# Kernel optimization log

Measured on AMD Instinct MI355X. Metric: run time of the kernel, lower is better.

The kernel has to match this reference:

```python
import jax, jax.numpy as jnp
import numpy as np
from jax import lax

BN_EPS = 1e-3
SLOPE = 0.1
CLUSTER_TEMP = 30.0
K = 16
FEAT = 4096  # 8*8*64


def conv_bn_lrelu(x, w, b, g, beta, m, v):
    # Conv2d stride 2, padding 1 (NCHW / OIHW), then eval-mode BatchNorm, then LeakyReLU.
    y = lax.conv_general_dilated(x, w, window_strides=(2, 2), padding=((1, 1), (1, 1)),
                                 dimension_numbers=("NCHW", "OIHW", "NCHW"))
    y = y + b[None, :, None, None]
    scale = g / jnp.sqrt(v + BN_EPS)
    y = y * scale[None, :, None, None] + (beta - m * scale)[None, :, None, None]
    return jnp.where(y > 0, y, SLOPE * y)


def soft_kmeans(data, mu, num_iter, ct):
    # Row L2-normalize (equivalent to diag(1/||x||) @ data)
    data = data / jnp.linalg.norm(data, axis=1, keepdims=True)
    for _ in range(num_iter):
        dist = data @ mu.T                      # [N, K]
        r = jax.nn.softmax(ct * dist, axis=1)   # [N, K]
        mu = (r.T @ data) / r.sum(axis=0)[:, None]  # [K, F]
    dist = data @ mu.T
    r = jax.nn.softmax(ct * dist, axis=1)
    return mu, r, dist


def setup_inputs() -> dict:
    key = jax.random.key(0)
    ks = jax.random.split(key, 12)
    d = {}
    d["x"] = jax.random.normal(ks[0], (256, 3, 64, 64), dtype=jnp.float32)
    # conv1: 3 -> 128
    d["conv1_w"] = jax.random.normal(ks[1], (128, 3, 3, 3), dtype=jnp.float32) * 0.05
    d["conv1_b"] = jnp.zeros((128,), jnp.float32)
    d["bn1_g"] = jnp.ones((128,), jnp.float32)
    d["bn1_b"] = jnp.zeros((128,), jnp.float32)
    d["bn1_m"] = jax.random.normal(ks[2], (128,), dtype=jnp.float32) * 0.1
    d["bn1_v"] = jax.random.uniform(ks[3], (128,), minval=0.5, maxval=1.5, dtype=jnp.float32)
    # conv2: 128 -> 256
    d["conv2_w"] = jax.random.normal(ks[4], (256, 128, 3, 3), dtype=jnp.float32) * 0.02
    d["conv2_b"] = jnp.zeros((256,), jnp.float32)
    d["bn2_g"] = jnp.ones((256,), jnp.float32)
    d["bn2_b"] = jnp.zeros((256,), jnp.float32)
    d["bn2_m"] = jax.random.normal(ks[5], (256,), dtype=jnp.float32) * 0.1
    d["bn2_v"] = jax.random.uniform(ks[6], (256,), minval=0.5, maxval=1.5, dtype=jnp.float32)
    # conv3: 256 -> 64
    d["conv3_w"] = jax.random.normal(ks[7], (64, 256, 3, 3), dtype=jnp.float32) * 0.02
    d["conv3_b"] = jnp.zeros((64,), jnp.float32)
    d["bn3_g"] = jnp.ones((64,), jnp.float32)
    d["bn3_b"] = jnp.zeros((64,), jnp.float32)
    d["bn3_m"] = jax.random.normal(ks[8], (64,), dtype=jnp.float32) * 0.1
    d["bn3_v"] = jax.random.uniform(ks[9], (64,), minval=0.5, maxval=1.5, dtype=jnp.float32)
    # initial cluster centers, torch.rand(K, F)
    d["mu0"] = jax.random.uniform(ks[10], (K, FEAT), dtype=jnp.float32)
    d["num_iter"] = 10
    return d


def reference(x, conv1_w, conv1_b, bn1_g, bn1_b, bn1_m, bn1_v,
              conv2_w, conv2_b, bn2_g, bn2_b, bn2_m, bn2_v,
              conv3_w, conv3_b, bn3_g, bn3_b, bn3_m, bn3_v,
              mu0, num_iter):
    h = conv_bn_lrelu(x, conv1_w, conv1_b, bn1_g, bn1_b, bn1_m, bn1_v)   # [B,128,32,32]
    h = conv_bn_lrelu(h, conv2_w, conv2_b, bn2_g, bn2_b, bn2_m, bn2_v)   # [B,256,16,16]
    h = conv_bn_lrelu(h, conv3_w, conv3_b, bn3_g, bn3_b, bn3_m, bn3_v)   # [B,64,8,8]
    embeds = h.reshape(-1, FEAT)                                          # [B, 4096]
    mu_init, _, _ = soft_kmeans(embeds, mu0, num_iter, CLUSTER_TEMP)
    _, r, _ = soft_kmeans(embeds, lax.stop_gradient(mu_init), 1, CLUSTER_TEMP)
    return r
```

## Files before the change

### kernel.cpp

```cpp
#include <hip/hip_runtime.h>
#include <stdint.h>
#include <stddef.h>

typedef unsigned short u16;
typedef __attribute__((ext_vector_type(8))) short short8;
typedef __attribute__((ext_vector_type(4))) float f32x4;
typedef __attribute__((ext_vector_type(4))) int int4v;

__device__ __forceinline__ float bf2f(u16 u) {
    unsigned x = ((unsigned)u) << 16;
    return __uint_as_float(x);
}
__device__ __forceinline__ u16 f2bf(float f) {
    unsigned x = __float_as_uint(f);
    unsigned r = (x + 0x7fffu + ((x >> 16) & 1u)) >> 16;
    return (u16)r;
}
__device__ __forceinline__ float ldin(const void* p, size_t i, int isbf) {
    return isbf ? bf2f(((const u16*)p)[i]) : ((const float*)p)[i];
}
__device__ __forceinline__ int detect_bf(const void* v1) {
    const u16* ub = (const u16*)v1;
    int ok = 1;
#pragma unroll
    for (int i = 0; i < 16; i++) {
        float f = bf2f(ub[i]);
        if (!(f >= 0.4f && f <= 1.6f)) ok = 0;
    }
    return ok;
}
__device__ __forceinline__ int sw(int r, int c8) {
    return r * 32 + (((c8) ^ (r & 3)) << 3);
}

struct PrepArgs {
    const void *w1, *w2, *w3;
    u16 *W1p, *W2p, *W3p;
    const void *b1, *g1, *be1, *m1, *v1;
    const void *b2, *g2, *be2, *m2, *v2;
    const void *b3, *g3, *be3, *m3, *v3;
    float *es1, *esh1, *es2, *esh2, *es3, *esh3;
    u16 *zb;
};
__device__ __forceinline__ void packw_body(const void* src, u16* dst, int CI, int Kp,
                                           int total, int blk, int t, int isbf) {
    int p = blk * 256 + t;
    if (p >= total) return;
    int co = p / Kp, k = p - co * Kp;
    int tap = k / CI, ci = k - tap * CI;
    u16 v = 0;
    if (tap < 9) {
        size_t si = (size_t)(co * CI + ci) * 9 + tap;
        v = isbf ? ((const u16*)src)[si] : f2bf(((const float*)src)[si]);
    }
    dst[p] = v;
}
__global__ __launch_bounds__(256) void kprep_all(PrepArgs A) {
    int b = blockIdx.x, t = threadIdx.x;
    int isbf = detect_bf(A.v1);
    if (b < 1152) {
        packw_body(A.w2, A.W2p, 128, 1152, 256 * 1152, b, t, isbf);
    } else if (b < 1728) {
        packw_body(A.w3, A.W3p, 256, 2304, 64 * 2304, b - 1152, t, isbf);
    } else if (b < 1744) {
        packw_body(A.w1, A.W1p, 3, 32, 128 * 32, b - 1728, t, isbf);
    } else {
        if (b == 1745) A.zb[t] = 0;
        int u = (b - 1744) * 256 + t;
        const void *bb, *g, *be, *m, *v;
        float *es, *esh;
        int c;
        if (u < 128)      { c = u;       bb=A.b1; g=A.g1; be=A.be1; m=A.m1; v=A.v1; es=A.es1; esh=A.esh1; }
        else if (u < 384) { c = u - 128; bb=A.b2; g=A.g2; be=A.be2; m=A.m2; v=A.v2; es=A.es2; esh=A.esh2; }
        else if (u < 448) { c = u - 384; bb=A.b3; g=A.g3; be=A.be3; m=A.m3; v=A.v3; es=A.es3; esh=A.esh3; }
        else return;
        float sc = ldin(g, c, isbf) / sqrtf(ldin(v, c, isbf) + 1e-3f);
        float sh = (ldin(bb, c, isbf) - ldin(m, c, isbf)) * sc + ldin(be, c, isbf);
        es[c] = sc;
        esh[c] = sh;
    }
}

__global__ void kfallback(u16* __restrict__ out) {
    int i = blockIdx.x * 256 + threadIdx.x;
    if (i < 4096) out[i] = f2bf(0.0625f);
}

__global__ __launch_bounds__(256) void im2col1(const void* __restrict__ x,
                                               u16* __restrict__ A1,
                                               const void* __restrict__ v1ref) {
    int n = blockIdx.x, t = threadIdx.x;
    int isbf = detect_bf(v1ref);
    __shared__ u16 xs[3 * 64 * 64];
    if (isbf) {
        const u16* xp = (const u16*)x + (size_t)n * 12288;
#pragma unroll
        for (int i = t * 8; i < 12288; i += 2048)
            *(int4v*)&xs[i] = *(const int4v*)&xp[i];
    } else {
        const float* xp = (const float*)x + (size_t)n * 12288;
#pragma unroll
        for (int i = t * 4; i < 12288; i += 1024) {
            float4 v = *(const float4*)&xp[i];
            xs[i] = f2bf(v.x); xs[i + 1] = f2bf(v.y);
            xs[i + 2] = f2bf(v.z); xs[i + 3] = f2bf(v.w);
        }
    }
    __syncthreads();
#pragma unroll
    for (int rr = 0; rr < 4; rr++) {
        int m = rr * 256 + t;
        int ox = m & 31, oy = m >> 5;
        alignas(16) u16 row[32];
#pragma unroll
        for (int k = 0; k < 32; k++) {
            u16 val = 0;
            if (k < 27) {
                int tap = k / 3, ci = k - 3 * tap;
                int ky = tap / 3, kx = tap - 3 * ky;
                int iy = 2 * oy - 1 + ky, ix = 2 * ox - 1 + kx;
                if ((unsigned)iy < 64u && (unsigned)ix < 64u)
                    val = xs[ci * 4096 + iy * 64 + ix];
            }
            row[k] = val;
        }
        int4v* dst = (int4v*)(A1 + ((size_t)n * 1024 + m) * 32);
        const int4v* srcv = (const int4v*)row;
#pragma unroll
        for (int q = 0; q < 4; q++) dst[q] = srcv[q];
    }
}

__global__ __launch_bounds__(256) void gemm_conv1(
    const u16* __restrict__ A1, const u16* __restrict__ W,
    const float* __restrict__ es, const float* __restrict__ esh,
    u16* __restrict__ OutB) {
    alignas(16) __shared__ u16 As[128 * 32];
    alignas(16) __shared__ u16 Bs[128 * 32];
    const int t = threadIdx.x;
    const int m0 = blockIdx.x * 128;
    const int lane = t & 63, w = t >> 6;
    const int wm = w & 1, wn = w >> 1;
    const int rA = t >> 2, c8 = t & 3, koff = c8 * 8;

#pragma unroll
    for (int j = 0; j < 2; j++) {
        int4v va = *(const int4v*)(A1 + (size_t)(m0 + j * 64 + rA) * 32 + koff);
        *(int4v*)&As[sw(j * 64 + rA, c8)] = va;
        int4v vb = *(const int4v*)(W + (size_t)(j * 64 + rA) * 32 + koff);
        *(int4v*)&Bs[sw(j * 64 + rA, c8)] = vb;
    }
    __syncthreads();
    const int qc = lane >> 4, fr = lane & 15;
    short8 af[4], bf[4];
#pragma unroll
    for (int i = 0; i < 4; i++) af[i] = *(const short8*)&As[sw(wm * 64 + i * 16 + fr, qc)];
#pragma unroll
    for (int j = 0; j < 4; j++) bf[j] = *(const short8*)&Bs[sw(wn * 64 + j * 16 + fr, qc)];
    f32x4 acc[4][4];
#pragma unroll
    for (int i = 0; i < 4; i++)
#pragma unroll
        for (int j = 0; j < 4; j++) {
#pragma unroll
            for (int q = 0; q < 4; q++) acc[i][j][q] = 0.f;
            acc[i][j] = __builtin_amdgcn_mfma_f32_16x16x32_bf16(af[i], bf[j], acc[i][j], 0, 0, 0);
        }
    float scv[4], shv[4];
#pragma unroll
    for (int j = 0; j < 4; j++) {
        int c = wn * 64 + j * 16 + fr;
        scv[j] = es[c];
        shv[j] = esh[c];
    }
#pragma unroll
    for (int i = 0; i < 4; i++) {
#pragma unroll
        for (int rg = 0; rg < 4; rg++) {
            int m = m0 + wm * 64 + i * 16 + qc * 4 + rg;
            int ox = m & 31, oy = (m >> 5) & 31, n = m >> 10;
            u16* orow = OutB + ((size_t)(n * 32 + oy) * 32 + ox) * 128 + wn * 64 + fr;
#pragma unroll
            for (int j = 0; j < 4; j++) {
                float v = acc[i][j][rg] * scv[j] + shv[j];
                v = (v > 0.f) ? v : 0.1f * v;
                orow[j * 16] = f2bf(v);
            }
        }
    }
}

__global__ __launch_bounds__(512, 2) void gemm_conv2(
    const u16* __restrict__ h1, const u16* __restrict__ W,
    const float* __restrict__ es, const float* __restrict__ esh,
    u16* __restrict__ OutB, const u16* __restrict__ zb) {
    alignas(16) __shared__ u16 smem[4 * 16384];
    u16* const Ab0 = smem;
    u16* const Ab1 = smem + 16384;
    u16* const Bb0 = smem + 32768;
    u16* const Bb1 = smem + 49152;

    const int t = threadIdx.x;
    const int w = t >> 6, l = t & 63;
    const int img = blockIdx.x;
    const int wm = w >> 2, wn = w & 3;
    const int fr = l & 15, qc = l >> 4;

    int aiy0[4], aix0[4], ac8e[4];
    int brow[4];
#pragma unroll
    for (int i = 0; i < 4; ++i) {
        int gi = w * 256 + i * 64 + l;
        int r = gi >> 3, c8d = gi & 7;
        int c8s = c8d ^ (r & 7);
        int oy = r >> 4, ox = r & 15;
        aiy0[i] = 2 * oy - 1;
        aix0[i] = 2 * ox - 1;
        ac8e[i] = c8s * 8;
        brow[i] = r * 1152 + c8s * 8;
    }
    auto mkA = [&](int i, int ky, int kx) -> const u16* {
        int iy = aiy0[i] + ky, ix = aix0[i] + kx;
        if ((unsigned)iy < 32u && (unsigned)ix < 32u)
            return h1 + (size_t)(((img * 32 + iy) * 32 + ix) * 128 + ac8e[i]);
        return zb;
    };
    auto stage = [&](const u16* src, u16* ldsbase, int i) {
        __builtin_amdgcn_global_load_lds(
            (const __attribute__((address_space(1))) void*)src,
            (__attribute__((address_space(3))) void*)(ldsbase + (w * 4 + i) * 512),
            16, 0, 0);
    };

    f32x4 acc[8][4];
#pragma unroll
    for (int mi = 0; mi < 8; ++mi)
#pragma unroll
        for (int nj = 0; nj < 4; ++nj)
#pragma unroll
            for (int q = 0; q < 4; ++q) acc[mi][nj][q] = 0.0f;

    auto do_tile = [&](const u16* A, const u16* B) {
#pragma unroll
        for (int kk = 0; kk < 2; ++kk) {
            const int c8 = kk * 4 + qc;
            short8 a[8], b[4];
#pragma unroll
            for (int q = 0; q < 8; ++q) {
                int row = wm * 128 + q * 16 + fr;
                a[q] = *(const short8*)(A + row * 64 + ((c8 ^ (row & 7)) << 3));
            }
#pragma unroll
            for (int j = 0; j < 4; ++j) {
                int row = wn * 64 + j * 16 + fr;
                b[j] = *(const short8*)(B + row * 64 + ((c8 ^ (row & 7)) << 3));
            }
            __builtin_amdgcn_s_setprio(1);
#pragma unroll
            for (int q = 0; q < 8; ++q)
#pragma unroll
                for (int j = 0; j < 4; ++j)
                    acc[q][j] = __builtin_amdgcn_mfma_f32_16x16x32_bf16(
                        a[q], b[j], acc[q][j], 0, 0, 0);
            __builtin_amdgcn_s_setprio(0);
        }
    };

    const u16* pcur[4];
#pragma unroll
    for (int i = 0; i < 4; ++i) pcur[i] = mkA(i, 0, 0);
#pragma unroll
    for (int i = 0; i < 4; ++i) {
        stage(pcur[i], Ab0, i);
        stage(W + brow[i], Bb0, i);
    }

    for (int tap = 0; tap < 9; ++tap) {
        __syncthreads();
#pragma unroll
        for (int i = 0; i < 4; ++i) {
            stage(pcur[i] + 64, Ab1, i);
            stage(W + brow[i] + (2 * tap + 1) * 64, Bb1, i);
        }
        do_tile(Ab0, Bb0);
        __syncthreads();
        if (tap < 8) {
            const int tap2 = tap + 1;
            const int ky2 = (tap2 >= 6) ? 2 : (tap2 >= 3) ? 1 : 0;
            const int kx2 = tap2 - 3 * ky2;
#pragma unroll
            for (int i = 0; i < 4; ++i) pcur[i] = mkA(i, ky2, kx2);
#pragma unroll
            for (int i = 0; i < 4; ++i) {
                stage(pcur[i], Ab0, i);
                stage(W + brow[i] + (2 * tap + 2) * 64, Bb0, i);
            }
        }
        do_tile(Ab1, Bb1);
    }

    float scv[4], shv[4];
#pragma unroll
    for (int nj = 0; nj < 4; ++nj) {
        int c = wn * 64 + nj * 16 + fr;
        scv[nj] = es[c];
        shv[nj] = esh[c];
    }
#pragma unroll
    for (int mi = 0; mi < 8; ++mi) {
#pragma unroll
        for (int rg = 0; rg < 4; ++rg) {
            int r = wm * 128 + mi * 16 + qc * 4 + rg;
            u16* orow = OutB + ((size_t)img * 256 + r) * 256 + wn * 64 + fr;
#pragma unroll
            for (int nj = 0; nj < 4; ++nj) {
                float v = acc[mi][nj][rg] * scv[nj] + shv[nj];
                v = (v > 0.f) ? v : 0.1f * v;
                orow[nj * 16] = f2bf(v);
            }
        }
    }
}

__global__ __launch_bounds__(256) void gemm_conv3f(
    const u16* __restrict__ Asrc, const u16* __restrict__ W,
    const float* __restrict__ es3, const float* __restrict__ esh3,
    float* __restrict__ dat, u16* __restrict__ datbf,
    const u16* __restrict__ zb) {
    alignas(16) __shared__ u16 smem[4 * 4096];
    __shared__ float red[4];
    u16* const AbP[2] = {smem, smem + 4096};
    u16* const BbP[2] = {smem + 8192, smem + 12288};

    const int t = threadIdx.x;
    const int w = t >> 6, l = t & 63;
    const int lid = blockIdx.x;
    const int xcd = lid & 7, slot = lid >> 3;
    const int img = xcd * 32 + slot;
    const int wm = w & 1, wn = w >> 1;
    const int fr = l & 15, qc = l >> 4;

    int aiy0[2], aix0[2], ac8e[2];
    int brow[2];
#pragma unroll
    for (int i = 0; i < 2; ++i) {
        int g = w * 128 + i * 64 + l;
        int r = g >> 3, c8d = g & 7;
        int c8s = c8d ^ (r & 7);
        int oy = r >> 3, ox = r & 7;
        aiy0[i] = 2 * oy - 1;
        aix0[i] = 2 * ox - 1;
        ac8e[i] = c8s * 8;
        brow[i] = r * 2304 + c8s * 8;
    }
    auto mkA = [&](int i, int ky, int kx) -> const u16* {
        int iy = aiy0[i] + ky, ix = aix0[i] + kx;
        if ((unsigned)iy < 16u && (unsigned)ix < 16u)
            return Asrc + (size_t)(((img * 16 + iy) * 16 + ix) * 256 + ac8e[i]);
        return zb;
    };
    auto stage = [&](const u16* src, u16* ldsbase, int i) {
        __builtin_amdgcn_global_load_lds(
            (const __attribute__((address_space(1))) void*)src,
            (__attribute__((address_space(3))) void*)(ldsbase + (w * 2 + i) * 512),
            16, 0, 0);
    };

    f32x4 acc[2][2];
#pragma unroll
    for (int i = 0; i < 2; i++)
#pragma unroll
        for (int j = 0; j < 2; j++)
#pragma unroll
            for (int q = 0; q < 4; q++) acc[i][j][q] = 0.0f;

    auto do_tile = [&](const u16* A, const u16* B) {
#pragma unroll
        for (int kk = 0; kk < 2; ++kk) {
            const int c8 = kk * 4 + qc;
            short8 a[2], b[2];
#pragma unroll
            for (int i = 0; i < 2; ++i) {
                int row = wm * 32 + i * 16 + fr;
                a[i] = *(const short8*)(A + row * 64 + ((c8 ^ (row & 7)) << 3));
            }
#pragma unroll
            for (int j = 0; j < 2; ++j) {
                int row = wn * 32 + j * 16 + fr;
                b[j] = *(const short8*)(B + row * 64 + ((c8 ^ (row & 7)) << 3));
            }
            __builtin_amdgcn_s_setprio(1);
#pragma unroll
            for (int i = 0; i < 2; ++i)
#pragma unroll
                for (int j = 0; j < 2; ++j)
                    acc[i][j] = __builtin_amdgcn_mfma_f32_16x16x32_bf16(
                        a[i], b[j], acc[i][j], 0, 0, 0);
            __builtin_amdgcn_s_setprio(0);
        }
    };

    const u16* pcur[2];
#pragma unroll
    for (int i = 0; i < 2; ++i) pcur[i] = mkA(i, 0, 0);
#pragma unroll
    for (int i = 0; i < 2; ++i) {
        stage(pcur[i], AbP[0], i);
        stage(W + brow[i], BbP[0], i);
    }

    int flat = 0;
    for (int tap = 0; tap < 9; ++tap) {
        for (int q4 = 0; q4 < 4; ++q4, ++flat) {
            const int cb = flat & 1;
            __syncthreads();
            int ntap = tap, nq = q4 + 1;
            if (nq == 4) { nq = 0; ntap = tap + 1; }
            if (ntap < 9) {
                if (nq == 0) {
                    const int ky = (ntap >= 6) ? 2 : (ntap >= 3) ? 1 : 0;
                    const int kx = ntap - 3 * ky;
#pragma unroll
                    for (int i = 0; i < 2; ++i) pcur[i] = mkA(i, ky, kx);
                }
#pragma unroll
                for (int i = 0; i < 2; ++i) {
                    stage(pcur[i] + nq * 64, AbP[cb ^ 1], i);
                    stage(W + brow[i] + ntap * 256 + nq * 64, BbP[cb ^ 1], i);
                }
            }
            do_tile(AbP[cb], BbP[cb]);
        }
    }

    float vals[2][2][4];
    float ssq = 0.f;
#pragma unroll
    for (int j = 0; j < 2; j++) {
        int c = wn * 32 + j * 16 + fr;
        float sc = es3[c], sh = esh3[c];
#pragma unroll
        for (int i = 0; i < 2; i++) {
#pragma unroll
            for (int rg = 0; rg < 4; rg++) {
                float v = acc[i][j][rg] * sc + sh;
                v = (v > 0.f) ? v : 0.1f * v;
                vals[i][j][rg] = v;
                ssq += v * v;
            }
        }
    }
#pragma unroll
    for (int off = 32; off > 0; off >>= 1) ssq += __shfl_xor(ssq, off);
    if (l == 0) red[w] = ssq;
    __syncthreads();
    float inv = 1.0f / sqrtf(red[0] + red[1] + red[2] + red[3]);
#pragma unroll
    for (int j = 0; j < 2; j++) {
        int c = wn * 32 + j * 16 + fr;
#pragma unroll
        for (int i = 0; i < 2; i++) {
#pragma unroll
            for (int rg = 0; rg < 4; rg++) {
                int row = wm * 32 + i * 16 + qc * 4 + rg;
                size_t idx = (size_t)img * 4096 + c * 64 + row;
                float v = vals[i][j][rg] * inv;
                dat[idx] = v;
                datbf[idx] = f2bf(v);
            }
        }
    }
}

__global__ __launch_bounds__(256) void kgr(const u16* __restrict__ dbf,
                                           const float* __restrict__ dat,
                                           const void* __restrict__ mu0,
                                           float* __restrict__ Gp,
                                           float* __restrict__ rb0,
                                           const void* __restrict__ v1ref) {
    const int b = blockIdx.x, t = threadIdx.x;
    __shared__ float part[16][4];
    __shared__ float ds[16];

    if (b < 64) {
        const int tile = b & 15, s = b >> 4;
        const int m0 = (tile & 3) * 64, n0 = (tile >> 2) * 64;
        const int lane = t & 63, w = t >> 6;
        const int wm = w & 1, wn = w >> 1;
        const int fr = lane & 15, qc = lane >> 4;

        f32x4 acc[2][2];
#pragma unroll
        for (int i = 0; i < 2; i++)
#pragma unroll
            for (int j = 0; j < 2; j++)
#pragma unroll
                for (int q = 0; q < 4; q++) acc[i][j][q] = 0.0f;

        const u16* a0p = dbf + (size_t)(m0 + wm * 32 + fr) * 4096 + s * 1024 + qc * 8;
        const u16* a1p = a0p + 16 * 4096;
        const u16* b0p = dbf + (size_t)(n0 + wn * 32 + fr) * 4096 + s * 1024 + qc * 8;
        const u16* b1p = b0p + 16 * 4096;

        short8 Pa0[4], Pa1[4], Pb0[4], Pb1[4];
        short8 Qa0[4], Qa1[4], Qb0[4], Qb1[4];
        auto ldc = [&](short8* A0, short8* A1, short8* B0, short8* B1, int c) {
#pragma unroll
            for (int u = 0; u < 4; ++u) {
                const int o = c * 128 + u * 32;
                A0[u] = *(const short8*)(a0p + o);
                A1[u] = *(const short8*)(a1p + o);
                B0[u] = *(const short8*)(b0p + o);
                B1[u] = *(const short8*)(b1p + o);
            }
        };
        auto mmc = [&](short8* A0, short8* A1, short8* B0, short8* B1) {
#pragma unroll
            for (int u = 0; u < 4; ++u) {
                acc[0][0] = __builtin_amdgcn_mfma_f32_16x16x32_bf16(A0[u], B0[u], acc[0][0], 0, 0, 0);
                acc[0][1] = __builtin_amdgcn_mfma_f32_16x16x32_bf16(A0[u], B1[u], acc[0][1], 0, 0, 0);
                acc[1][0] = __builtin_amdgcn_mfma_f32_16x16x32_bf16(A1[u], B0[u], acc[1][0], 0, 0, 0);
                acc[1][1] = __builtin_amdgcn_mfma_f32_16x16x32_bf16(A1[u], B1[u], acc[1][1], 0, 0, 0);
            }
        };
        ldc(Pa0, Pa1, Pb0, Pb1, 0);
#pragma unroll
        for (int c = 0; c < 4; ++c) {
            ldc(Qa0, Qa1, Qb0, Qb1, 2 * c + 1);
            mmc(Pa0, Pa1, Pb0, Pb1);
            if (c < 3) ldc(Pa0, Pa1, Pb0, Pb1, 2 * c + 2);
            mmc(Qa0, Qa1, Qb0, Qb1);
        }

        float* gp = Gp + (size_t)s * 65536;
#pragma unroll
        for (int j = 0; j < 2; j++) {
            int cc = n0 + wn * 32 + j * 16 + fr;
#pragma unroll
            for (int i = 0; i < 2; i++)
#pragma unroll
                for (int rg = 0; rg < 4; rg++) {
                    int row = m0 + wm * 32 + i * 16 + qc * 4 + rg;
                    gp[row * 256 + cc] = acc[i][j][rg];
                }
        }
    } else {
        const int n = b - 64;
        const int isbf = detect_bf(v1ref);
        const int lane = t & 63, wv = t >> 6;
        float d[16];
#pragma unroll
        for (int j = 0; j < 16; j++) d[j] = dat[(size_t)n * 4096 + j * 256 + t];
#pragma unroll
        for (int k = 0; k < 16; k++) {
            float a = 0.f;
            if (isbf) {
                const u16* mp = (const u16*)mu0 + (size_t)k * 4096;
#pragma unroll
                for (int j = 0; j < 16; j++) a = fmaf(d[j], bf2f(mp[j * 256 + t]), a);
            } else {
                const float* mp = (const float*)mu0 + (size_t)k * 4096;
#pragma unroll
                for (int j = 0; j < 16; j++) a = fmaf(d[j], mp[j * 256 + t], a);
            }
#pragma unroll
            for (int off = 32; off > 0; off >>= 1) a += __shfl_xor(a, off);
            if (lane == 0) part[k][wv] = a;
        }
        __syncthreads();
        if (t < 16) {
            float dk = part[t][0] + part[t][1] + part[t][2] + part[t][3];
            ds[t] = dk;
            __syncthreads();
            float mx = -1e30f;
#pragma unroll
            for (int j = 0; j < 16; j++) mx = fmaxf(mx, ds[j]);
            float sum = 0.f;
#pragma unroll
            for (int j = 0; j < 16; j++) sum += __expf(30.f * (ds[j] - mx));
            rb0[n * 16 + t] = __expf(30.f * (dk - mx)) / sum;
        }
    }
}

__global__ __launch_bounds__(256) void kcomb(const float* __restrict__ Gp,
                                             u16* __restrict__ Ghi,
                                             u16* __restrict__ Glo) {
    const int i = (blockIdx.x * 256 + threadIdx.x) * 4;
    f32x4 s0 = *(const f32x4*)(Gp + i);
    f32x4 s1 = *(const f32x4*)(Gp + 65536 + i);
    f32x4 s2 = *(const f32x4*)(Gp + 131072 + i);
    f32x4 s3 = *(const f32x4*)(Gp + 196608 + i);
    unsigned long long ph = 0, pl = 0;
#pragma unroll
    for (int q = 0; q < 4; q++) {
        float v = ((s0[q] + s1[q]) + s2[q]) + s3[q];
        u16 hi = f2bf(v);
        u16 lo = f2bf(v - bf2f(hi));
        ph |= ((unsigned long long)hi) << (16 * q);
        pl |= ((unsigned long long)lo) << (16 * q);
    }
    *(unsigned long long*)(Ghi + i) = ph;
    *(unsigned long long*)(Glo + i) = pl;
}

__global__ __launch_bounds__(1024) void kmiter(const u16* __restrict__ Ghi,
                                               const u16* __restrict__ Glo,
                                               const float* __restrict__ rb0,
                                               void* __restrict__ dout,
                                               const void* __restrict__ v1ref) {
    const int t = threadIdx.x;
    const int isbf = detect_bf(v1ref);
    const int lane = t & 63, w = t >> 6;
    const int i0 = w * 16;
    const int col = lane & 15;
    const int q = lane >> 4;

    __shared__ u16 rThi[2][16 * 264];
    __shared__ u16 rTlo[2][16 * 264];
    __shared__ float part[2][16][17];

    const u16* Ahirow = Ghi + (size_t)(i0 + col) * 256 + q * 8;
    const u16* Alorow = Glo + (size_t)(i0 + col) * 256 + q * 8;

    {
        float rv[4];
#pragma unroll
        for (int rg = 0; rg < 4; rg++) {
            int row = i0 + q * 4 + rg;
            float v = rb0[row * 16 + col];
            rv[rg] = v;
            u16 hi = f2bf(v);
            rThi[0][col * 264 + row] = hi;
            rTlo[0][col * 264 + row] = f2bf(v - bf2f(hi));
        }
        float s0 = rv[0] + rv[1] + rv[2] + rv[3];
        s0 += __shfl_xor(s0, 16);
        s0 += __shfl_xor(s0, 32);
        if (lane < 16) part[0][w][lane] = s0;
    }
    __syncthreads();
    float rsc = 0.f;
#pragma unroll
    for (int ww = 0; ww < 16; ww++) rsc += part[0][ww][col];

    int cur = 0;
    for (int iter = 0; iter < 11; iter++) {
        f32x4 acc0 = {0.f, 0.f, 0.f, 0.f};
        f32x4 acc1 = {0.f, 0.f, 0.f, 0.f};
#pragma unroll
        for (int s = 0; s < 4; s++) {
            {
                short8 ah = *(const short8*)(Ahirow + s * 32);
                short8 al = *(const short8*)(Alorow + s * 32);
                short8 bh = *(const short8*)&rThi[cur][col * 264 + s * 32 + q * 8];
                short8 bl = *(const short8*)&rTlo[cur][col * 264 + s * 32 + q * 8];
                acc0 = __builtin_amdgcn_mfma_f32_16x16x32_bf16(ah, bh, acc0, 0, 0, 0);
                acc0 = __builtin_amdgcn_mfma_f32_16x16x32_bf16(al, bh, acc0, 0, 0, 0);
                acc0 = __builtin_amdgcn_mfma_f32_16x16x32_bf16(ah, bl, acc0, 0, 0, 0);
            }
            {
                short8 ah = *(const short8*)(Ahirow + (s + 4) * 32);
                short8 al = *(const short8*)(Alorow + (s + 4) * 32);
                short8 bh = *(const short8*)&rThi[cur][col * 264 + (s + 4) * 32 + q * 8];
                short8 bl = *(const short8*)&rTlo[cur][col * 264 + (s + 4) * 32 + q * 8];
                acc1 = __builtin_amdgcn_mfma_f32_16x16x32_bf16(ah, bh, acc1, 0, 0, 0);
                acc1 = __builtin_amdgcn_mfma_f32_16x16x32_bf16(al, bh, acc1, 0, 0, 0);
                acc1 = __builtin_amdgcn_mfma_f32_16x16x32_bf16(ah, bl, acc1, 0, 0, 0);
            }
        }
        float nv[4];
#pragma unroll
        for (int rg = 0; rg < 4; rg++) {
            float dk = (acc0[rg] + acc1[rg]) / rsc;
            float mx = dk;
#pragma unroll
            for (int o = 1; o < 16; o <<= 1) mx = fmaxf(mx, __shfl_xor(mx, o));
            float e = __expf(30.f * (dk - mx));
            float ssum = e;
#pragma unroll
            for (int o = 1; o < 16; o <<= 1) ssum += __shfl_xor(ssum, o);
            nv[rg] = e / ssum;
        }
        if (iter < 10) {
            const int nxt = cur ^ 1;
#pragma unroll
            for (int rg = 0; rg < 4; rg++) {
                int row = i0 + q * 4 + rg;
                u16 hi = f2bf(nv[rg]);
                rThi[nxt][col * 264 + row] = hi;
                rTlo[nxt][col * 264 + row] = f2bf(nv[rg] - bf2f(hi));
            }
            float s0 = nv[0] + nv[1] + nv[2] + nv[3];
            s0 += __shfl_xor(s0, 16);
            s0 += __shfl_xor(s0, 32);
            if (lane < 16) part[nxt][w][lane] = s0;
            __syncthreads();
            rsc = 0.f;
#pragma unroll
            for (int ww = 0; ww < 16; ww++) rsc += part[nxt][ww][col];
            cur = nxt;
        } else {
#pragma unroll
            for (int rg = 0; rg < 4; rg++) {
                int row = i0 + q * 4 + rg;
                if (isbf) ((u16*)dout)[row * 16 + col] = f2bf(nv[rg]);
                else ((float*)dout)[row * 16 + col] = nv[rg];
            }
        }
    }
}

extern "C" void kernel_launch(void* const* d_in, const int* in_sizes, int n_in,
                              void* d_out, int out_size, void* d_ws, size_t ws_size,
                              hipStream_t stream) {
    const void* x   = d_in[0];
    const void* w1  = d_in[1];
    const void* b1  = d_in[2];
    const void* g1  = d_in[3];
    const void* be1 = d_in[4];
    const void* m1  = d_in[5];
    const void* v1  = d_in[6];
    const void* w2  = d_in[7];
    const void* b2  = d_in[8];
    const void* g2  = d_in[9];
    const void* be2 = d_in[10];
    const void* m2  = d_in[11];
    const void* v2  = d_in[12];
    const void* w3  = d_in[13];
    const void* b3  = d_in[14];
    const void* g3  = d_in[15];
    const void* be3 = d_in[16];
    const void* m3  = d_in[17];
    const void* v3  = d_in[18];
    const void* mu0 = d_in[19];

    char* p = (char*)d_ws;
    size_t used = 0;
    auto alloc = [&](size_t bytes) -> char* {
        char* q = p;
        size_t rb = (bytes + 255) & ~(size_t)255;
        p += rb;
        used += rb;
        return q;
    };
    float* rb0 = (float*)alloc(4096 * 4);
    u16* Ghi = (u16*)alloc((size_t)65536 * 2);
    u16* Glo = (u16*)alloc((size_t)65536 * 2);
    float* Gp = (float*)alloc((size_t)4 * 65536 * 4);
    u16* W1p = (u16*)alloc((size_t)128 * 32 * 2);
    u16* W2p = (u16*)alloc((size_t)256 * 1152 * 2);
    u16* W3p = (u16*)alloc((size_t)64 * 2304 * 2);
    float* es1 = (float*)alloc(128 * 4);
    float* esh1 = (float*)alloc(128 * 4);
    float* es2 = (float*)alloc(256 * 4);
    float* esh2 = (float*)alloc(256 * 4);
    float* es3 = (float*)alloc(64 * 4);
    float* esh3 = (float*)alloc(64 * 4);
    u16* zb = (u16*)alloc(512);
    const size_t R1 = (size_t)256 * 32 * 32 * 128 * 2;
    const size_t R2 = (size_t)256 * 16 * 16 * 256 * 2;
    char* reg1 = alloc(R1);
    char* reg2 = alloc(R2);
    u16* h1 = (u16*)reg1;
    u16* A1 = (u16*)reg2;
    u16* h2 = (u16*)reg2;
    float* dat = (float*)reg1;
    u16* datbf = (u16*)(reg1 + 4194304);

    if (used > ws_size) {
        kfallback<<<16, 256, 0, stream>>>((u16*)d_out);
        return;
    }

    PrepArgs pa = {w1, w2, w3, W1p, W2p, W3p,
                   b1, g1, be1, m1, v1, b2, g2, be2, m2, v2, b3, g3, be3, m3, v3,
                   es1, esh1, es2, esh2, es3, esh3, zb};
    kprep_all<<<1746, 256, 0, stream>>>(pa);
    im2col1<<<256, 256, 0, stream>>>(x, A1, v1);
    gemm_conv1<<<dim3(2048), 256, 0, stream>>>(A1, W1p, es1, esh1, h1);
    gemm_conv2<<<dim3(256), 512, 0, stream>>>(h1, W2p, es2, esh2, h2, zb);
    gemm_conv3f<<<dim3(256), 256, 0, stream>>>(h2, W3p, es3, esh3, dat, datbf, zb);
    kgr<<<dim3(320), 256, 0, stream>>>(datbf, dat, mu0, Gp, rb0, v1);
    kcomb<<<dim3(64), 256, 0, stream>>>(Gp, Ghi, Glo);
    kmiter<<<1, 1024, 0, stream>>>(Ghi, Glo, rb0, d_out, v1);
}
```

Before: 257.6 us.

## Split Gram K-dimension 8 ways and register-cache Gram tiles in kmeans loop

The Gram-matrix kernel now splits the 4096-long reduction into 8 slices instead of 4, doubling the number of GEMM blocks to raise parallelism. The combine kernel sums 8 partials. The single-block kmeans iteration kernel drops from 1024 to 512 threads, each wave handling 32 rows. The Gram hi/lo fragments are loaded once into registers instead of being reloaded from global memory on every iteration, cutting repeated global loads on the serial critical path. The cost is more partial-sum traffic, higher register pressure, and half as many threads in the iteration kernel.

```diff
diff --git a/kernel.cpp b/kernel.cpp
--- a/kernel.cpp
+++ b/kernel.cpp
@@ -482,7 +482,7 @@
     __shared__ float part[16][4];
     __shared__ float ds[16];
 
-    if (b < 64) {
+    if (b < 128) {
         const int tile = b & 15, s = b >> 4;
         const int m0 = (tile & 3) * 64, n0 = (tile >> 2) * 64;
         const int lane = t & 63, w = t >> 6;
@@ -497,9 +497,9 @@
 #pragma unroll
                 for (int q = 0; q < 4; q++) acc[i][j][q] = 0.0f;
 
-        const u16* a0p = dbf + (size_t)(m0 + wm * 32 + fr) * 4096 + s * 1024 + qc * 8;
+        const u16* a0p = dbf + (size_t)(m0 + wm * 32 + fr) * 4096 + s * 512 + qc * 8;
         const u16* a1p = a0p + 16 * 4096;
-        const u16* b0p = dbf + (size_t)(n0 + wn * 32 + fr) * 4096 + s * 1024 + qc * 8;
+        const u16* b0p = dbf + (size_t)(n0 + wn * 32 + fr) * 4096 + s * 512 + qc * 8;
         const u16* b1p = b0p + 16 * 4096;
 
         short8 Pa0[4], Pa1[4], Pb0[4], Pb1[4];
@@ -525,10 +525,10 @@
         };
         ldc(Pa0, Pa1, Pb0, Pb1, 0);
 #pragma unroll
-        for (int c = 0; c < 4; ++c) {
+        for (int c = 0; c < 2; ++c) {
             ldc(Qa0, Qa1, Qb0, Qb1, 2 * c + 1);
             mmc(Pa0, Pa1, Pb0, Pb1);
-            if (c < 3) ldc(Pa0, Pa1, Pb0, Pb1, 2 * c + 2);
+            if (c < 1) ldc(Pa0, Pa1, Pb0, Pb1, 2 * c + 2);
             mmc(Qa0, Qa1, Qb0, Qb1);
         }
 
@@ -545,7 +545,7 @@
                 }
         }
     } else {
-        const int n = b - 64;
+        const int n = b - 128;
         const int isbf = detect_bf(v1ref);
         const int lane = t & 63, wv = t >> 6;
         float d[16];
@@ -587,14 +587,15 @@
                                              u16* __restrict__ Ghi,
                                              u16* __restrict__ Glo) {
     const int i = (blockIdx.x * 256 + threadIdx.x) * 4;
-    f32x4 s0 = *(const f32x4*)(Gp + i);
-    f32x4 s1 = *(const f32x4*)(Gp + 65536 + i);
-    f32x4 s2 = *(const f32x4*)(Gp + 131072 + i);
-    f32x4 s3 = *(const f32x4*)(Gp + 196608 + i);
+    f32x4 s[8];
+#pragma unroll
+    for (int p = 0; p < 8; p++) s[p] = *(const f32x4*)(Gp + (size_t)p * 65536 + i);
     unsigned long long ph = 0, pl = 0;
 #pragma unroll
     for (int q = 0; q < 4; q++) {
-        float v = ((s0[q] + s1[q]) + s2[q]) + s3[q];
+        float v = s[0][q];
+#pragma unroll
+        for (int p = 1; p < 8; p++) v += s[p][q];
         u16 hi = f2bf(v);
         u16 lo = f2bf(v - bf2f(hi));
         ph |= ((unsigned long long)hi) << (16 * q);
@@ -604,37 +605,49 @@
     *(unsigned long long*)(Glo + i) = pl;
 }
 
-__global__ __launch_bounds__(1024) void kmiter(const u16* __restrict__ Ghi,
-                                               const u16* __restrict__ Glo,
-                                               const float* __restrict__ rb0,
-                                               void* __restrict__ dout,
-                                               const void* __restrict__ v1ref) {
+__global__ __launch_bounds__(512) void kmiter(const u16* __restrict__ Ghi,
+                                              const u16* __restrict__ Glo,
+                                              const float* __restrict__ rb0,
+                                              void* __restrict__ dout,
+                                              const void* __restrict__ v1ref) {
     const int t = threadIdx.x;
     const int isbf = detect_bf(v1ref);
     const int lane = t & 63, w = t >> 6;
-    const int i0 = w * 16;
+    const int i0 = w * 32;
     const int col = lane & 15;
     const int q = lane >> 4;
 
     __shared__ u16 rThi[2][16 * 264];
     __shared__ u16 rTlo[2][16 * 264];
-    __shared__ float part[2][16][17];
-
-    const u16* Ahirow = Ghi + (size_t)(i0 + col) * 256 + q * 8;
-    const u16* Alorow = Glo + (size_t)(i0 + col) * 256 + q * 8;
+    __shared__ float part[2][8][17];
+
+    short8 gh[2][8], gl[2][8];
+#pragma unroll
+    for (int sg = 0; sg < 2; sg++) {
+        const u16* Ah = Ghi + (size_t)(i0 + sg * 16 + col) * 256 + q * 8;
+        const u16* Al = Glo + (size_t)(i0 + sg * 16 + col) * 256 + q * 8;
+#pragma unroll
+        for (int s = 0; s < 8; s++) {
+            gh[sg][s] = *(const short8*)(Ah + s * 32);
+            gl[sg][s] = *(const short8*)(Al + s * 32);
+        }
+    }
 
     {
-        float rv[4];
-#pragma unroll
-        for (int rg = 0; rg < 4; rg++) {
-            int row = i0 + q * 4 + rg;
-            float v = rb0[row * 16 + col];
-            rv[rg] = v;
-            u16 hi = f2bf(v);
-            rThi[0][col * 264 + row] = hi;
-            rTlo[0][col * 264 + row] = f2bf(v - bf2f(hi));
-        }
-        float s0 = rv[0] + rv[1] + rv[2] + rv[3];
+        float rv[2][4];
+#pragma unroll
+        for (int sg = 0; sg < 2; sg++)
+#pragma unroll
+            for (int rg = 0; rg < 4; rg++) {
+                int row = i0 + sg * 16 + q * 4 + rg;
+                float v = rb0[row * 16 + col];
+                rv[sg][rg] = v;
+                u16 hi = f2bf(v);
+                rThi[0][col * 264 + row] = hi;
+                rTlo[0][col * 264 + row] = f2bf(v - bf2f(hi));
+            }
+        float s0 = (rv[0][0] + rv[0][1] + rv[0][2] + rv[0][3]) +
+                   (rv[1][0] + rv[1][1] + rv[1][2] + rv[1][3]);
         s0 += __shfl_xor(s0, 16);
         s0 += __shfl_xor(s0, 32);
         if (lane < 16) part[0][w][lane] = s0;
@@ -642,71 +655,76 @@
     __syncthreads();
     float rsc = 0.f;
 #pragma unroll
-    for (int ww = 0; ww < 16; ww++) rsc += part[0][ww][col];
+    for (int ww = 0; ww < 8; ww++) rsc += part[0][ww][col];
 
     int cur = 0;
     for (int iter = 0; iter < 11; iter++) {
-        f32x4 acc0 = {0.f, 0.f, 0.f, 0.f};
-        f32x4 acc1 = {0.f, 0.f, 0.f, 0.f};
+        f32x4 a0[2] = {{0.f, 0.f, 0.f, 0.f}, {0.f, 0.f, 0.f, 0.f}};
+        f32x4 a1[2] = {{0.f, 0.f, 0.f, 0.f}, {0.f, 0.f, 0.f, 0.f}};
 #pragma unroll
         for (int s = 0; s < 4; s++) {
-            {
-                short8 ah = *(const short8*)(Ahirow + s * 32);
-                short8 al = *(const short8*)(Alorow + s * 32);
-                short8 bh = *(const short8*)&rThi[cur][col * 264 + s * 32 + q * 8];
-                short8 bl = *(const short8*)&rTlo[cur][col * 264 + s * 32 + q * 8];
-                acc0 = __builtin_amdgcn_mfma_f32_16x16x32_bf16(ah, bh, acc0, 0, 0, 0);
-                acc0 = __builtin_amdgcn_mfma_f32_16x16x32_bf16(al, bh, acc0, 0, 0, 0);
-                acc0 = __builtin_amdgcn_mfma_f32_16x16x32_bf16(ah, bl, acc0, 0, 0, 0);
-            }
-            {
-                short8 ah = *(const short8*)(Ahirow + (s + 4) * 32);
-                short8 al = *(const short8*)(Alorow + (s + 4) * 32);
-                short8 bh = *(const short8*)&rThi[cur][col * 264 + (s + 4) * 32 + q * 8];
-                short8 bl = *(const short8*)&rTlo[cur][col * 264 + (s + 4) * 32 + q * 8];
-                acc1 = __builtin_amdgcn_mfma_f32_16x16x32_bf16(ah, bh, acc1, 0, 0, 0);
-                acc1 = __builtin_amdgcn_mfma_f32_16x16x32_bf16(al, bh, acc1, 0, 0, 0);
-                acc1 = __builtin_amdgcn_mfma_f32_16x16x32_bf16(ah, bl, acc1, 0, 0, 0);
-            }
-        }
-        float nv[4];
-#pragma unroll
-        for (int rg = 0; rg < 4; rg++) {
-            float dk = (acc0[rg] + acc1[rg]) / rsc;
-            float mx = dk;
-#pragma unroll
-            for (int o = 1; o < 16; o <<= 1) mx = fmaxf(mx, __shfl_xor(mx, o));
-            float e = __expf(30.f * (dk - mx));
-            float ssum = e;
-#pragma unroll
-            for (int o = 1; o < 16; o <<= 1) ssum += __shfl_xor(ssum, o);
-            nv[rg] = e / ssum;
-        }
+            short8 bh = *(const short8*)&rThi[cur][col * 264 + s * 32 + q * 8];
+            short8 bl = *(const short8*)&rTlo[cur][col * 264 + s * 32 + q * 8];
+#pragma unroll
+            for (int sg = 0; sg < 2; sg++) {
+                a0[sg] = __builtin_amdgcn_mfma_f32_16x16x32_bf16(gh[sg][s], bh, a0[sg], 0, 0, 0);
+                a0[sg] = __builtin_amdgcn_mfma_f32_16x16x32_bf16(gl[sg][s], bh, a0[sg], 0, 0, 0);
+                a0[sg] = __builtin_amdgcn_mfma_f32_16x16x32_bf16(gh[sg][s], bl, a0[sg], 0, 0, 0);
+            }
+            short8 bh2 = *(const short8*)&rThi[cur][col * 264 + (s + 4) * 32 + q * 8];
+            short8 bl2 = *(const short8*)&rTlo[cur][col * 264 + (s + 4) * 32 + q * 8];
+#pragma unroll
+            for (int sg = 0; sg < 2; sg++) {
+                a1[sg] = __builtin_amdgcn_mfma_f32_16x16x32_bf16(gh[sg][s + 4], bh2, a1[sg], 0, 0, 0);
+                a1[sg] = __builtin_amdgcn_mfma_f32_16x16x32_bf16(gl[sg][s + 4], bh2, a1[sg], 0, 0, 0);
+                a1[sg] = __builtin_amdgcn_mfma_f32_16x16x32_bf16(gh[sg][s + 4], bl2, a1[sg], 0, 0, 0);
+            }
+        }
+        float nv[2][4];
+#pragma unroll
+        for (int sg = 0; sg < 2; sg++)
+#pragma unroll
+            for (int rg = 0; rg < 4; rg++) {
+                float dk = (a0[sg][rg] + a1[sg][rg]) / rsc;
+                float mx = dk;
+#pragma unroll
+                for (int o = 1; o < 16; o <<= 1) mx = fmaxf(mx, __shfl_xor(mx, o));
+                float e = __expf(30.f * (dk - mx));
+                float ssum = e;
+#pragma unroll
+                for (int o = 1; o < 16; o <<= 1) ssum += __shfl_xor(ssum, o);
+                nv[sg][rg] = e / ssum;
+            }
         if (iter < 10) {
             const int nxt = cur ^ 1;
 #pragma unroll
-            for (int rg = 0; rg < 4; rg++) {
-                int row = i0 + q * 4 + rg;
-                u16 hi = f2bf(nv[rg]);
-                rThi[nxt][col * 264 + row] = hi;
-                rTlo[nxt][col * 264 + row] = f2bf(nv[rg] - bf2f(hi));
-            }
-            float s0 = nv[0] + nv[1] + nv[2] + nv[3];
+            for (int sg = 0; sg < 2; sg++)
+#pragma unroll
+                for (int rg = 0; rg < 4; rg++) {
+                    int row = i0 + sg * 16 + q * 4 + rg;
+                    u16 hi = f2bf(nv[sg][rg]);
+                    rThi[nxt][col * 264 + row] = hi;
+                    rTlo[nxt][col * 264 + row] = f2bf(nv[sg][rg] - bf2f(hi));
+                }
+            float s0 = (nv[0][0] + nv[0][1] + nv[0][2] + nv[0][3]) +
+                       (nv[1][0] + nv[1][1] + nv[1][2] + nv[1][3]);
             s0 += __shfl_xor(s0, 16);
             s0 += __shfl_xor(s0, 32);
             if (lane < 16) part[nxt][w][lane] = s0;
             __syncthreads();
             rsc = 0.f;
 #pragma unroll
-            for (int ww = 0; ww < 16; ww++) rsc += part[nxt][ww][col];
+            for (int ww = 0; ww < 8; ww++) rsc += part[nxt][ww][col];
             cur = nxt;
         } else {
 #pragma unroll
-            for (int rg = 0; rg < 4; rg++) {
-                int row = i0 + q * 4 + rg;
-                if (isbf) ((u16*)dout)[row * 16 + col] = f2bf(nv[rg]);
-                else ((float*)dout)[row * 16 + col] = nv[rg];
-            }
+            for (int sg = 0; sg < 2; sg++)
+#pragma unroll
+                for (int rg = 0; rg < 4; rg++) {
+                    int row = i0 + sg * 16 + q * 4 + rg;
+                    if (isbf) ((u16*)dout)[row * 16 + col] = f2bf(nv[sg][rg]);
+                    else ((float*)dout)[row * 16 + col] = nv[sg][rg];
+                }
         }
     }
 }
@@ -747,7 +765,7 @@
     float* rb0 = (float*)alloc(4096 * 4);
     u16* Ghi = (u16*)alloc((size_t)65536 * 2);
     u16* Glo = (u16*)alloc((size_t)65536 * 2);
-    float* Gp = (float*)alloc((size_t)4 * 65536 * 4);
+    float* Gp = (float*)alloc((size_t)8 * 65536 * 4);
     u16* W1p = (u16*)alloc((size_t)128 * 32 * 2);
     u16* W2p = (u16*)alloc((size_t)256 * 1152 * 2);
     u16* W3p = (u16*)alloc((size_t)64 * 2304 * 2);
@@ -781,7 +799,7 @@
     gemm_conv1<<<dim3(2048), 256, 0, stream>>>(A1, W1p, es1, esh1, h1);
     gemm_conv2<<<dim3(256), 512, 0, stream>>>(h1, W2p, es2, esh2, h2, zb);
     gemm_conv3f<<<dim3(256), 256, 0, stream>>>(h2, W3p, es3, esh3, dat, datbf, zb);
-    kgr<<<dim3(320), 256, 0, stream>>>(datbf, dat, mu0, Gp, rb0, v1);
+    kgr<<<dim3(384), 256, 0, stream>>>(datbf, dat, mu0, Gp, rb0, v1);
     kcomb<<<dim3(64), 256, 0, stream>>>(Gp, Ghi, Glo);
-    kmiter<<<1, 1024, 0, stream>>>(Ghi, Glo, rb0, d_out, v1);
-}
+    kmiter<<<1, 512, 0, stream>>>(Ghi, Glo, rb0, d_out, v1);
+}
```

After: 247.0 us. 1.04x faster.
